# Optimization experiments

Hardware: AMD Instinct MI355X
Metric: run time of the kernel (lower is better)

## Reference

```python
import jax, jax.numpy as jnp
import numpy as np

B, D_INNER, D_STATE, DT_RANK = 512, 5120, 16, 160


def setup_inputs() -> dict:
    key = jax.random.key(0)
    ks = jax.random.split(key, 9)
    s = lambda fan: 1.0 / np.sqrt(fan)
    x = jax.random.normal(ks[0], (B, 1, 1, D_INNER), dtype=jnp.float32)
    W_dt_rank = jax.random.normal(ks[1], (DT_RANK, D_INNER), dtype=jnp.float32) * s(D_INNER)
    W_dt = jax.random.normal(ks[2], (D_INNER, DT_RANK), dtype=jnp.float32) * s(DT_RANK)
    b_dt = jax.random.normal(ks[3], (D_INNER,), dtype=jnp.float32)
    W_B = jax.random.normal(ks[4], (D_STATE, D_INNER), dtype=jnp.float32) * s(D_INNER)
    W_C = jax.random.normal(ks[5], (D_STATE, D_INNER), dtype=jnp.float32) * s(D_INNER)
    # A = -exp(A_log) as in preprocess_A; keep entries negative
    A = -jnp.exp(jax.random.normal(ks[6], (D_INNER, D_STATE), dtype=jnp.float32) * 0.5)
    D = jax.random.normal(ks[7], (D_INNER,), dtype=jnp.float32)
    h = jax.random.normal(ks[8], (B, D_INNER, D_STATE), dtype=jnp.float32) * 0.1
    return {"x": x, "W_dt_rank": W_dt_rank, "W_dt": W_dt, "b_dt": b_dt,
            "W_B": W_B, "W_C": W_C, "A": A, "D": D, "h": h}


def reference(x, W_dt_rank, W_dt, b_dt, W_B, W_C, A, D, h):
    # x: [B,1,1,d_inner] -> [B,d_inner]
    xf = x.reshape(B, D_INNER)
    # delta_t: low-rank dt projection + dt_proj + softplus -> [B,d_inner]
    dt = jax.nn.softplus(jnp.einsum('br,dr->bd', jnp.einsum('bd,rd->br', xf, W_dt_rank), W_dt) + b_dt)
    Bc = jnp.einsum('bd,sd->bs', xf, W_B)  # [B,d_state]
    Cc = jnp.einsum('bd,sd->bs', xf, W_C)  # [B,d_state]
    # delta_A = exp(A * dt), broadcast dt over d_state  -> [B,d_inner,d_state]
    dA = jnp.exp(A[None, :, :] * dt[:, :, None])
    # delta_B = dt * B, broadcast B over d_inner -> [B,d_inner,d_state]
    dB = dt[:, :, None] * Bc[:, None, :]
    # hidden state update
    h_new = dA * h + dB * xf[:, :, None]
    # y = h_new @ C + D * x  -> [B,d_inner]
    y = jnp.einsum('bds,bs->bd', h_new, Cc) + D[None, :] * xf
    return y.reshape(B, 1, 1, D_INNER)
```

## Files before the change

kernel.cpp:

```cpp
#include <hip/hip_runtime.h>
#include <math.h>

#define BATCH 512
#define DIN   5120
#define DST   16
#define RK    160
#define NJ    192
#define NZ1   16

typedef __attribute__((ext_vector_type(8))) __bf16 bf16x8;
typedef __attribute__((ext_vector_type(4))) float f32x4;
typedef __attribute__((ext_vector_type(8))) unsigned short ushort8;

#define OFF_XP    0u
#define OFF_WP    5242880u
#define OFF_WDTP  7208960u
#define OFF_PART  8847360u
#define OFF_DTRP  15138816u
#define OFF_B     15302656u
#define OFF_C     15335424u

__device__ __forceinline__ unsigned short f2bf(float f) {
  unsigned int u = __float_as_uint(f);
  u = (u + 0x7FFFu + ((u >> 16) & 1u)) >> 16;
  return (unsigned short)u;
}

__global__ __launch_bounds__(256) void k_prep2(
    const float* __restrict__ x, const float* __restrict__ Wdtr,
    const float* __restrict__ WB, const float* __restrict__ WC,
    const float* __restrict__ Wdt, char* __restrict__ ws)
{
  __shared__ unsigned short sT[64 * 264];
  const int t = threadIdx.x;
  const int bid = blockIdx.x;

  if (bid < 160) {
    const int bt = bid & 7, kt = bid >> 3;
    const int b0 = bt * 64, k0 = kt * 256;
#pragma unroll
    for (int i = 0; i < 16; ++i) {
      const int f = i * 256 + t;
      const int r = f >> 6, c = f & 63;
      const float4 v = *(const float4*)&x[(size_t)(b0 + r) * DIN + k0 + c * 4];
      unsigned short* p = &sT[r * 264 + c * 4];
      p[0] = f2bf(v.x); p[1] = f2bf(v.y); p[2] = f2bf(v.z); p[3] = f2bf(v.w);
    }
    __syncthreads();
    ushort8* xP = (ushort8*)(ws + OFF_XP);
#pragma unroll
    for (int i = 0; i < 8; ++i) {
      const int o = i * 256 + t;
      const int k8l = o >> 6, bl = o & 63;
      const unsigned short* p = &sT[bl * 264 + k8l * 8];
      ushort8 v;
#pragma unroll
      for (int e = 0; e < 8; ++e) v[e] = p[e];
      xP[(size_t)(kt * 32 + k8l) * 512 + b0 + bl] = v;
    }
  } else if (bid < 220) {
    const int bb = bid - 160;
    const int jt = bb % 3, kt = bb / 3;
    const int j0 = jt * 64, k0 = kt * 256;
#pragma unroll
    for (int i = 0; i < 16; ++i) {
      const int f = i * 256 + t;
      const int r = f >> 6, c = f & 63;
      const int j = j0 + r;
      const float* row;
      if (j < RK)            row = Wdtr + (size_t)j * DIN;
      else if (j < RK + DST) row = WB   + (size_t)(j - RK) * DIN;
      else                   row = WC   + (size_t)(j - RK - DST) * DIN;
      const float4 v = *(const float4*)&row[k0 + c * 4];
      unsigned short* p = &sT[r * 264 + c * 4];
      p[0] = f2bf(v.x); p[1] = f2bf(v.y); p[2] = f2bf(v.z); p[3] = f2bf(v.w);
    }
    __syncthreads();
    ushort8* WPo = (ushort8*)(ws + OFF_WP);
#pragma unroll
    for (int i = 0; i < 8; ++i) {
      const int o = i * 256 + t;
      const int k8l = o >> 6, jl = o & 63;
      const unsigned short* p = &sT[jl * 264 + k8l * 8];
      ushort8 v;
#pragma unroll
      for (int e = 0; e < 8; ++e) v[e] = p[e];
      WPo[(size_t)(kt * 32 + k8l) * 192 + j0 + jl] = v;
    }
  } else {
    const int d0 = (bid - 220) * 64;
#pragma unroll
    for (int i = 0; i < 10; ++i) {
      const int f = i * 256 + t;
      const int r = f / 40, c = f - r * 40;
      const float4 v = *(const float4*)&Wdt[(size_t)(d0 + r) * RK + c * 4];
      unsigned short* p = &sT[r * 168 + c * 4];
      p[0] = f2bf(v.x); p[1] = f2bf(v.y); p[2] = f2bf(v.z); p[3] = f2bf(v.w);
    }
    __syncthreads();
    ushort8* WdtPo = (ushort8*)(ws + OFF_WDTP);
#pragma unroll
    for (int i = 0; i < 5; ++i) {
      const int o = i * 256 + t;
      const int k8l = o >> 6, dl = o & 63;
      const unsigned short* p = &sT[dl * 168 + k8l * 8];
      ushort8 v;
#pragma unroll
      for (int e = 0; e < 8; ++e) v[e] = p[e];
      WdtPo[(size_t)k8l * 5120 + d0 + dl] = v;
    }
  }
}

__global__ __launch_bounds__(256) void k_g1(char* __restrict__ ws)
{
  const int wid  = blockIdx.x * 4 + (threadIdx.x >> 6);
  const int l    = threadIdx.x & 63;
  const int z    = wid / 384;
  const int rem  = wid - z * 384;
  const int jt   = rem >> 5;
  const int bt   = rem & 31;
  const int j0   = jt * 16, b0 = bt * 16;

  const bf16x8* WPv = (const bf16x8*)(ws + OFF_WP);
  const bf16x8* xPv = (const bf16x8*)(ws + OFF_XP);
  float* part = (float*)(ws + OFF_PART);

  const int lg = l >> 4, lr = l & 15;
  f32x4 acc = {0.f, 0.f, 0.f, 0.f};

#pragma unroll 2
  for (int s = 0; s < 10; ++s) {
    const int k8 = z * 40 + s * 4 + lg;
    const bf16x8 av = WPv[(size_t)k8 * 192 + j0 + lr];
    const bf16x8 bv = xPv[(size_t)k8 * 512 + b0 + lr];
    acc = __builtin_amdgcn_mfma_f32_16x16x32_bf16(av, bv, acc, 0, 0, 0);
  }

  float* pb = part + (size_t)wid * 256;
#pragma unroll
  for (int r = 0; r < 4; ++r)
    pb[(lg * 4 + r) * 16 + lr] = acc[r];
}

__global__ __launch_bounds__(256) void k_red1(char* __restrict__ ws)
{
  const int e = blockIdx.x * 256 + threadIdx.x;
  const int j = e >> 9, b = e & 511;
  const int jt = j >> 4, jr = j & 15, bt = b >> 4, bc = b & 15;

  const float* part = (const float*)(ws + OFF_PART);
  float s = 0.f;
#pragma unroll
  for (int z = 0; z < NZ1; ++z)
    s += part[((size_t)(z * 384 + jt * 32 + bt) << 8) + jr * 16 + bc];

  if (j < RK) {
    unsigned short* dtrP = (unsigned short*)(ws + OFF_DTRP);
    dtrP[((size_t)(j >> 3) * 512 + b) * 8 + (j & 7)] = f2bf(s);
  } else if (j < RK + DST) {
    ((float*)(ws + OFF_B))[(size_t)b * DST + (j - RK)] = s;
  } else {
    ((float*)(ws + OFF_C))[(size_t)b * DST + (j - RK - DST)] = s;
  }
}

__global__ __launch_bounds__(256) void k_g2y(
    const float* __restrict__ bdt, const float* __restrict__ A,
    const float* __restrict__ Dp,  const float* __restrict__ x,
    const float* __restrict__ h,   float* __restrict__ y,
    char* __restrict__ ws)
{
  __shared__ float sDT[4][16][17];
  __shared__ float sB[4][16][16];
  __shared__ float sC[4][16][16];
  __shared__ float sX[4][16][16];

  const int w = threadIdx.x >> 6;
  const int l = threadIdx.x & 63;
  const int wid = blockIdx.x * 4 + w;
  const int dtile = wid % 320, btile = wid / 320;
  const int d0 = dtile * 16, b0 = btile * 16;

  const bf16x8* dtrPv = (const bf16x8*)(ws + OFF_DTRP);
  const bf16x8* WdtPv = (const bf16x8*)(ws + OFF_WDTP);
  const float*  Bc    = (const float*)(ws + OFF_B);
  const float*  Cc    = (const float*)(ws + OFF_C);

  *(float4*)&((float*)sB[w])[l * 4] = *(const float4*)&Bc[b0 * DST + l * 4];
  *(float4*)&((float*)sC[w])[l * 4] = *(const float4*)&Cc[b0 * DST + l * 4];
  {
    const int xr = l >> 2, xc = (l & 3) * 4;
    *(float4*)&sX[w][xr][xc] = *(const float4*)&x[(size_t)(b0 + xr) * DIN + d0 + xc];
  }

  const int lg = l >> 4, lr = l & 15;
  f32x4 acc = {0.f, 0.f, 0.f, 0.f};
#pragma unroll
  for (int s = 0; s < 5; ++s) {
    const int k8 = s * 4 + lg;
    const bf16x8 av = dtrPv[(size_t)k8 * 512 + b0 + lr];
    const bf16x8 bv = WdtPv[(size_t)k8 * 5120 + d0 + lr];
    acc = __builtin_amdgcn_mfma_f32_16x16x32_bf16(av, bv, acc, 0, 0, 0);
  }
  const float bias = bdt[d0 + lr];
#pragma unroll
  for (int r = 0; r < 4; ++r) {
    const float pre = acc[r] + bias;
    sDT[w][lg * 4 + r][lr] = (pre > 20.f) ? pre : log1pf(__expf(pre));
  }
  __syncthreads();

  const int q = l & 3;
  const int Q = l >> 2;
  const int d = d0 + Q;
  const float4 A4 = *(const float4*)(A + (size_t)d * DST + q * 4);
  const float  Dv = Dp[d];

  const float* hp = h + ((size_t)b0 * DIN + d) * DST + q * 4;
  float* yp = y + (size_t)b0 * DIN + d;

  float4 hbuf[4];
#pragma unroll
  for (int j = 0; j < 4; ++j)
    hbuf[j] = *(const float4*)(hp + (size_t)j * (DIN * DST));

#pragma unroll
  for (int j = 0; j < 16; ++j) {
    const float4 h4 = hbuf[j & 3];
    if (j + 4 < 16)
      hbuf[j & 3] = *(const float4*)(hp + (size_t)(j + 4) * (DIN * DST));

    const float dtv = sDT[w][j][Q];
    const float xv  = sX[w][j][Q];
    const float dtx = dtv * xv;
    const float4 B4 = *(const float4*)&sB[w][j][q * 4];
    const float4 C4 = *(const float4*)&sC[w][j][q * 4];

    const float dA0 = __expf(A4.x * dtv);
    const float dA1 = __expf(A4.y * dtv);
    const float dA2 = __expf(A4.z * dtv);
    const float dA3 = __expf(A4.w * dtv);
    const float hn0 = fmaf(dA0, h4.x, dtx * B4.x);
    const float hn1 = fmaf(dA1, h4.y, dtx * B4.y);
    const float hn2 = fmaf(dA2, h4.z, dtx * B4.z);
    const float hn3 = fmaf(dA3, h4.w, dtx * B4.w);
    float p = hn0 * C4.x + hn1 * C4.y + hn2 * C4.z + hn3 * C4.w;

    p += __shfl_xor(p, 1);
    p += __shfl_xor(p, 2);
    if (q == 0) yp[(size_t)j * DIN] = fmaf(Dv, xv, p);
  }
}

extern "C" void kernel_launch(void* const* d_in, const int* in_sizes, int n_in,
                              void* d_out, int out_size, void* d_ws, size_t ws_size,
                              hipStream_t stream) {
  const float* x    = (const float*)d_in[0];
  const float* Wdtr = (const float*)d_in[1];
  const float* Wdt  = (const float*)d_in[2];
  const float* bdt  = (const float*)d_in[3];
  const float* WB   = (const float*)d_in[4];
  const float* WC   = (const float*)d_in[5];
  const float* A    = (const float*)d_in[6];
  const float* Dp   = (const float*)d_in[7];
  const float* h    = (const float*)d_in[8];
  float* y = (float*)d_out;
  char* ws = (char*)d_ws;

  k_prep2<<<dim3(300), 256, 0, stream>>>(x, Wdtr, WB, WC, Wdt, ws);
  k_g1<<<dim3(1536), 256, 0, stream>>>(ws);
  k_red1<<<dim3(384), 256, 0, stream>>>(ws);
  k_g2y<<<dim3(2560), 256, 0, stream>>>(bdt, A, Dp, x, h, y, ws);
}
```

Measured before the change: 55.93 us.

## Fuse split-K GEMM and partial-sum reduction into one kernel via shared memory

The first projection GEMM previously wrote 16 split-K partial tiles to global workspace and a separate kernel summed them. Now each 1024-thread block assigns the 16 K-slices to its 16 waves, reduces the accumulators in LDS, and writes the final dt-rank, B and C values directly. This removes one launch and the global round-trip of the partial buffer. In exchange it uses large blocks that need a block-wide barrier, and the grid drops to 384 blocks, which may reduce occupancy.

```diff
diff --git a/kernel.cpp b/kernel.cpp
--- a/kernel.cpp
+++ b/kernel.cpp
@@ -6,7 +6,6 @@
 #define DST   16
 #define RK    160
 #define NJ    192
-#define NZ1   16
 
 typedef __attribute__((ext_vector_type(8))) __bf16 bf16x8;
 typedef __attribute__((ext_vector_type(4))) float f32x4;
@@ -15,10 +14,9 @@
 #define OFF_XP    0u
 #define OFF_WP    5242880u
 #define OFF_WDTP  7208960u
-#define OFF_PART  8847360u
-#define OFF_DTRP  15138816u
-#define OFF_B     15302656u
-#define OFF_C     15335424u
+#define OFF_DTRP  8847360u
+#define OFF_B     9011200u
+#define OFF_C     9043968u
 
 __device__ __forceinline__ unsigned short f2bf(float f) {
   unsigned int u = __float_as_uint(f);
@@ -112,56 +110,50 @@
   }
 }
 
-__global__ __launch_bounds__(256) void k_g1(char* __restrict__ ws)
+__global__ __launch_bounds__(1024) void k_g1f2(char* __restrict__ ws)
 {
-  const int wid  = blockIdx.x * 4 + (threadIdx.x >> 6);
-  const int l    = threadIdx.x & 63;
-  const int z    = wid / 384;
-  const int rem  = wid - z * 384;
-  const int jt   = rem >> 5;
-  const int bt   = rem & 31;
-  const int j0   = jt * 16, b0 = bt * 16;
+  __shared__ float4 red[16][64];
+
+  const int t = threadIdx.x;
+  const int w = t >> 6, l = t & 63;
+  const int jt = blockIdx.x >> 5, bt = blockIdx.x & 31;
+  const int j0 = jt * 16, b0 = bt * 16;
 
   const bf16x8* WPv = (const bf16x8*)(ws + OFF_WP);
   const bf16x8* xPv = (const bf16x8*)(ws + OFF_XP);
-  float* part = (float*)(ws + OFF_PART);
 
   const int lg = l >> 4, lr = l & 15;
   f32x4 acc = {0.f, 0.f, 0.f, 0.f};
 
-#pragma unroll 2
+#pragma unroll
   for (int s = 0; s < 10; ++s) {
-    const int k8 = z * 40 + s * 4 + lg;
+    const int k8 = w * 40 + s * 4 + lg;
     const bf16x8 av = WPv[(size_t)k8 * 192 + j0 + lr];
     const bf16x8 bv = xPv[(size_t)k8 * 512 + b0 + lr];
     acc = __builtin_amdgcn_mfma_f32_16x16x32_bf16(av, bv, acc, 0, 0, 0);
   }
 
-  float* pb = part + (size_t)wid * 256;
-#pragma unroll
-  for (int r = 0; r < 4; ++r)
-    pb[(lg * 4 + r) * 16 + lr] = acc[r];
-}
-
-__global__ __launch_bounds__(256) void k_red1(char* __restrict__ ws)
-{
-  const int e = blockIdx.x * 256 + threadIdx.x;
-  const int j = e >> 9, b = e & 511;
-  const int jt = j >> 4, jr = j & 15, bt = b >> 4, bc = b & 15;
-
-  const float* part = (const float*)(ws + OFF_PART);
-  float s = 0.f;
-#pragma unroll
-  for (int z = 0; z < NZ1; ++z)
-    s += part[((size_t)(z * 384 + jt * 32 + bt) << 8) + jr * 16 + bc];
-
-  if (j < RK) {
-    unsigned short* dtrP = (unsigned short*)(ws + OFF_DTRP);
-    dtrP[((size_t)(j >> 3) * 512 + b) * 8 + (j & 7)] = f2bf(s);
-  } else if (j < RK + DST) {
-    ((float*)(ws + OFF_B))[(size_t)b * DST + (j - RK)] = s;
-  } else {
-    ((float*)(ws + OFF_C))[(size_t)b * DST + (j - RK - DST)] = s;
+  red[w][l] = (float4){acc[0], acc[1], acc[2], acc[3]};
+  __syncthreads();
+
+  if (t < 256) {
+    const int ll = t >> 2, r = t & 3;
+    const float* rp = (const float*)red;
+    float s = 0.f;
+#pragma unroll
+    for (int ww = 0; ww < 16; ++ww)
+      s += rp[(ww * 64 + ll) * 4 + r];
+
+    const int j = j0 + (ll >> 4) * 4 + r;
+    const int b = b0 + (ll & 15);
+    if (jt < 10) {
+      unsigned short* dtrP = (unsigned short*)(ws + OFF_DTRP);
+      dtrP[((size_t)(j >> 3) * 512 + b) * 8 + (j & 7)] = f2bf(s);
+    } else if (jt == 10) {
+      ((float*)(ws + OFF_B))[(size_t)b * DST + (j - 160)] = s;
+    } else {
+      ((float*)(ws + OFF_C))[(size_t)b * DST + (j - 176)] = s;
+    }
   }
 }
 
@@ -269,7 +261,6 @@
   char* ws = (char*)d_ws;
 
   k_prep2<<<dim3(300), 256, 0, stream>>>(x, Wdtr, WB, WC, Wdt, ws);
-  k_g1<<<dim3(1536), 256, 0, stream>>>(ws);
-  k_red1<<<dim3(384), 256, 0, stream>>>(ws);
+  k_g1f2<<<dim3(384), 1024, 0, stream>>>(ws);
   k_g2y<<<dim3(2560), 256, 0, stream>>>(bdt, A, Dp, x, h, y, ws);
 }
```

Result: faster. 54.14 us (-3.2%).
